# Kernel tuning notes

Measured on AMD Instinct MI355X. Metric: run time of the kernel, lower is better.

Reference implementation:

```python
import jax, jax.numpy as jnp
import numpy as np

NUM_GROUPS = 32
NUM_FEATURES = 256
EPS = 1e-5


def setup_inputs() -> dict:
    key = jax.random.key(0)
    x = jax.random.normal(key, (32, NUM_FEATURES, 64, 64), dtype=jnp.float32)
    gamma = jnp.ones((NUM_FEATURES,), jnp.float32)
    beta = jnp.zeros((NUM_FEATURES,), jnp.float32)
    return {"x": x, "gamma": gamma, "beta": beta}


def reference(x, gamma, beta):
    B, C, H, W = x.shape
    k = NUM_FEATURES // NUM_GROUPS  # channels per dynamic group
    # --- cosine similarity across channels (training path) ---
    x_flat = x.reshape(B, C, H * W)
    nrm = jnp.linalg.norm(x_flat, axis=2, keepdims=True)
    x_n = x_flat / jnp.maximum(nrm, 1e-12)  # F.normalize semantics
    cos = jnp.einsum('bcn,bdn->cd', x_n, x_n) / B  # mean over batch, [C,C]
    # torch.topk(|cos|, k, dim=0, largest=False): per-column k smallest.
    # Row c of |cos|.T is column c, so lax.top_k of -|cos|.T gives idx[c,i]=top_inds[i,c].
    _, idx = jax.lax.top_k(-jnp.abs(cos).T, k)  # [C, k]
    # --- group statistics without materializing [B,C,k,H,W] ---
    s = x.sum(axis=(2, 3))          # [B,C] per-channel spatial sum
    sq = (x * x).sum(axis=(2, 3))   # [B,C]
    # group = channel c itself + channels idx[c,1:]  (idx[:,0] replaced by x in original)
    gs = s + s[:, idx[:, 1:]].sum(axis=-1)    # [B,C]
    gsq = sq + sq[:, idx[:, 1:]].sum(axis=-1)  # [B,C]
    N = k * H * W
    mean = gs / N
    var = gsq / N - mean * mean  # unbiased=False
    inv = jax.lax.rsqrt(var + EPS)
    x_hat = (x - mean[:, :, None, None]) * inv[:, :, None, None]
    return gamma[None, :, None, None] * x_hat + beta[None, :, None, None]
```

## Files before the change

kernel.cpp:

```cpp
#include <hip/hip_runtime.h>
#include <math.h>

#define BATCH 32
#define CH 256
#define HW 4096
#define KSEL 8
#define EPSV 1e-5f

typedef __attribute__((ext_vector_type(8))) short short8;
typedef __attribute__((ext_vector_type(4))) float f32x4;

__global__ __launch_bounds__(1024) void gram256(const float* __restrict__ x,
                                                float* __restrict__ cosP,
                                                float* __restrict__ sP,
                                                float* __restrict__ sqP) {
    int z = blockIdx.x;
    int b = z >> 3, q = z & 7;
    const float* xb = x + (size_t)b * CH * HW;

    __shared__ unsigned short Hh[2][CH * 64];
    __shared__ unsigned short Hl[2][CH * 64];

    int t = threadIdx.x, lane = t & 63, w = t >> 6;
    int wr = (w >> 2) * 64, wc = (w & 3) * 64;
    int fr = lane & 15, fg = lane >> 4;

    int rowbase = t >> 4;
    int col16 = t & 15;
    int gr = col16 >> 1;
    int halfo = (col16 & 1) * 4;
    const float4* srcb4 = (const float4*)xb + (size_t)rowbase * (HW / 4) + q * 128 + col16;

    float sl[4] = {}, sql[4] = {};
    f32x4 acc[4][4] = {};
    float4 f[4];

#define LOAD4(KB) { const float4* sp = srcb4 + (size_t)(KB) * 16;                  \
    _Pragma("unroll") for (int i = 0; i < 4; ++i) f[i] = sp[(size_t)i * 65536]; }

#define CONVERT4(BUF) { _Pragma("unroll") for (int i = 0; i < 4; ++i) {            \
    float4 v = f[i];                                                               \
    sl[i] += v.x + v.y + v.z + v.w;                                                \
    sql[i] += v.x * v.x + v.y * v.y + v.z * v.z + v.w * v.w;                       \
    unsigned u0 = __float_as_uint(v.x), u1 = __float_as_uint(v.y);                 \
    unsigned u2 = __float_as_uint(v.z), u3 = __float_as_uint(v.w);                 \
    unsigned hp0 = (u0 >> 16) | (u1 & 0xffff0000u);                                \
    unsigned hp1 = (u2 >> 16) | (u3 & 0xffff0000u);                                \
    float lo0 = v.x - __uint_as_float(u0 & 0xffff0000u);                           \
    float lo1 = v.y - __uint_as_float(u1 & 0xffff0000u);                           \
    float lo2 = v.z - __uint_as_float(u2 & 0xffff0000u);                           \
    float lo3 = v.w - __uint_as_float(u3 & 0xffff0000u);                           \
    lo0 += lo0; lo1 += lo1; lo2 += lo2; lo3 += lo3;                                \
    unsigned lp0 = (__float_as_uint(lo0) >> 16) | (__float_as_uint(lo1) & 0xffff0000u); \
    unsigned lp1 = (__float_as_uint(lo2) >> 16) | (__float_as_uint(lo3) & 0xffff0000u); \
    int r = rowbase + 64 * i;                                                      \
    int adr = r * 64 + ((gr ^ (r & 7)) * 8) + halfo;                               \
    *(uint2*)&Hh[BUF][adr] = make_uint2(hp0, hp1);                                 \
    *(uint2*)&Hl[BUF][adr] = make_uint2(lp0, lp1);                                 \
} }

#define MFMA_PHASE(BUF) { _Pragma("unroll") for (int ks = 0; ks < 2; ++ks) {       \
    int gk = ks * 4 + fg;                                                          \
    short8 af[4], bb[4];                                                           \
    _Pragma("unroll") for (int mi = 0; mi < 4; ++mi) {                             \
        int r = wr + mi * 16 + fr;                                                 \
        af[mi] = *(const short8*)&Hh[BUF][r * 64 + ((gk ^ (r & 7)) * 8)];          \
    }                                                                              \
    _Pragma("unroll") for (int nj = 0; nj < 4; ++nj) {                             \
        int r = wc + nj * 16 + fr;                                                 \
        bb[nj] = *(const short8*)&Hh[BUF][r * 64 + ((gk ^ (r & 7)) * 8)];          \
    }                                                                              \
    _Pragma("unroll") for (int nj = 0; nj < 4; ++nj)                               \
        _Pragma("unroll") for (int mi = 0; mi < 4; ++mi)                           \
            acc[mi][nj] = __builtin_amdgcn_mfma_f32_16x16x32_bf16(af[mi], bb[nj], acc[mi][nj], 0, 0, 0); \
    _Pragma("unroll") for (int nj = 0; nj < 4; ++nj) {                             \
        int r = wc + nj * 16 + fr;                                                 \
        bb[nj] = *(const short8*)&Hl[BUF][r * 64 + ((gk ^ (r & 7)) * 8)];          \
    }                                                                              \
    _Pragma("unroll") for (int nj = 0; nj < 4; ++nj)                               \
        _Pragma("unroll") for (int mi = 0; mi < 4; ++mi)                           \
            acc[mi][nj] = __builtin_amdgcn_mfma_f32_16x16x32_bf16(af[mi], bb[nj], acc[mi][nj], 0, 0, 0); \
} }

    LOAD4(0)

#pragma unroll 1
    for (int kb = 0; kb < 8; ++kb) {
        CONVERT4(kb & 1)
        if (kb < 7) LOAD4(kb + 1)
        asm volatile("s_waitcnt lgkmcnt(0)" ::: "memory");
        __builtin_amdgcn_sched_barrier(0);
        __builtin_amdgcn_s_barrier();
        MFMA_PHASE(kb & 1)
    }

#pragma unroll
    for (int i = 0; i < 4; ++i) {
#pragma unroll
        for (int off = 1; off < 16; off <<= 1) {
            sl[i] += __shfl_xor(sl[i], off);
            sql[i] += __shfl_xor(sql[i], off);
        }
    }
    if ((t & 15) == 0) {
#pragma unroll
        for (int i = 0; i < 4; ++i) {
            int r = rowbase + 64 * i;
            sP[(size_t)z * CH + r] = sl[i];
            sqP[(size_t)z * CH + r] = sql[i];
        }
    }

    float* Cp = cosP + (size_t)z * CH * CH;
#pragma unroll
    for (int mi = 0; mi < 4; ++mi)
#pragma unroll
        for (int nj = 0; nj < 4; ++nj) {
#pragma unroll
            for (int reg = 0; reg < 4; ++reg) {
                int r = wr + mi * 16 + fg * 4 + reg;
                int c = wc + nj * 16 + fr;
                Cp[(size_t)r * CH + c] = acc[mi][nj][reg];
            }
        }
#undef LOAD4
#undef CONVERT4
#undef MFMA_PHASE
}

__global__ __launch_bounds__(256) void finalize_kernel(const float* __restrict__ sP,
                                                       const float* __restrict__ sqP,
                                                       float* __restrict__ s,
                                                       float* __restrict__ sq,
                                                       float* __restrict__ invn) {
    int b = blockIdx.x, c = threadIdx.x;
    float S = 0.f, Q = 0.f;
#pragma unroll
    for (int q = 0; q < 8; ++q) {
        S += sP[(size_t)(b * 8 + q) * CH + c];
        Q += sqP[(size_t)(b * 8 + q) * CH + c];
    }
    s[b * CH + c] = S;
    sq[b * CH + c] = Q;
    invn[b * CH + c] = 1.0f / fmaxf(sqrtf(Q), 1e-12f);
}

__global__ __launch_bounds__(1024) void reduceP(const float* __restrict__ cosP,
                                                const float* __restrict__ invn,
                                                float* __restrict__ R) {
    int r = blockIdx.x;
    int t = threadIdx.x;
    int d = t & 255, pg = t >> 8;
    const float* base = cosP + (size_t)r * CH + d;
    float acc = 0.f;
    for (int b = pg * 8; b < pg * 8 + 8; ++b) {
        float part = 0.f;
#pragma unroll
        for (int q = 0; q < 8; ++q)
            part += base[(size_t)(b * 8 + q) * (CH * CH)];
        acc += part * invn[b * CH + d] * invn[b * CH + r];
    }
    __shared__ float red[1024];
    red[t] = acc;
    __syncthreads();
    if (t < 256)
        R[(size_t)r * CH + t] = red[t] + red[t + 256] + red[t + 512] + red[t + 768];
}

__global__ __launch_bounds__(256) void symtopk(const float* __restrict__ R,
                                               int* __restrict__ idx) {
    int c = blockIdx.x;
    int d = threadIdx.x;
    float v = fabsf((R[(size_t)c * CH + d] + R[(size_t)d * CH + c]) * (0.5f / BATCH));

    __shared__ unsigned long long keys[CH];
    __shared__ unsigned long long wmin[4];
    __shared__ unsigned long long bmin;

    keys[d] = ((unsigned long long)__float_as_uint(v) << 32) | (unsigned)d;
    __syncthreads();

    for (int i = 0; i < KSEL; ++i) {
        unsigned long long k = keys[d];
        for (int off = 32; off; off >>= 1) {
            unsigned long long o = __shfl_down(k, off);
            k = (o < k) ? o : k;
        }
        if ((d & 63) == 0) wmin[d >> 6] = k;
        __syncthreads();
        if (d == 0) {
            unsigned long long m = wmin[0];
            if (wmin[1] < m) m = wmin[1];
            if (wmin[2] < m) m = wmin[2];
            if (wmin[3] < m) m = wmin[3];
            bmin = m;
            idx[c * KSEL + i] = (int)(m & 0xffffffffu);
        }
        __syncthreads();
        int sel = (int)(bmin & 0xffffffffu);
        if (d == sel) keys[d] = 0xffffffffffffffffULL;
        __syncthreads();
    }
}

__global__ __launch_bounds__(256) void groupstat_kernel(const float* __restrict__ s,
                                                        const float* __restrict__ sq,
                                                        const int* __restrict__ idx,
                                                        float* __restrict__ mean,
                                                        float* __restrict__ inv) {
    int b = blockIdx.x, c = threadIdx.x;
    float gs = s[b * CH + c], gq = sq[b * CH + c];
#pragma unroll
    for (int i = 1; i < KSEL; ++i) {
        int d = idx[c * KSEL + i];
        gs += s[b * CH + d];
        gq += sq[b * CH + d];
    }
    const float Ninv = 1.0f / (float)(KSEL * HW);
    float m = gs * Ninv;
    float var = gq * Ninv - m * m;
    mean[b * CH + c] = m;
    inv[b * CH + c]  = rsqrtf(var + EPSV);
}

__global__ __launch_bounds__(256) void norm_kernel(const float* __restrict__ x,
                                                   const float* __restrict__ mean,
                                                   const float* __restrict__ inv,
                                                   const float* __restrict__ gamma,
                                                   const float* __restrict__ beta,
                                                   float* __restrict__ out) {
    int i = blockIdx.x * 256 + threadIdx.x;
    int bc = i >> 10;
    int c  = bc & (CH - 1);
    float m = mean[bc], v = inv[bc];
    float g  = gamma[c] * v;
    float bt = beta[c] - m * g;
    float4 xv = ((const float4*)x)[i];
    float4 o;
    o.x = xv.x * g + bt;
    o.y = xv.y * g + bt;
    o.z = xv.z * g + bt;
    o.w = xv.w * g + bt;
    ((float4*)out)[i] = o;
}

extern "C" void kernel_launch(void* const* d_in, const int* in_sizes, int n_in,
                              void* d_out, int out_size, void* d_ws, size_t ws_size,
                              hipStream_t stream) {
    const float* x     = (const float*)d_in[0];
    const float* gamma = (const float*)d_in[1];
    const float* beta  = (const float*)d_in[2];
    float* out = (float*)d_out;

    float* cosP = (float*)d_out;

    float* ws   = (float*)d_ws;
    float* sP   = ws;
    float* sqP  = sP + 256 * CH;
    float* s    = sqP + 256 * CH;
    float* sq   = s + BATCH * CH;
    float* invn = sq + BATCH * CH;
    float* mean = invn + BATCH * CH;
    float* inv  = mean + BATCH * CH;
    float* R    = inv + BATCH * CH;
    int*   idx  = (int*)(R + CH * CH);

    gram256<<<256, 1024, 0, stream>>>(x, cosP, sP, sqP);
    finalize_kernel<<<BATCH, 256, 0, stream>>>(sP, sqP, s, sq, invn);
    reduceP<<<CH, 1024, 0, stream>>>(cosP, invn, R);
    symtopk<<<CH, 256, 0, stream>>>(R, idx);
    groupstat_kernel<<<BATCH, 256, 0, stream>>>(s, sq, idx, mean, inv);
    norm_kernel<<<(BATCH * CH * HW / 4) / 256, 256, 0, stream>>>(x, mean, inv, gamma, beta, out);
}
```

Measured before the change: 103.2 us.

## Stage gram inputs via global_load_lds double buffer with padded bf16 tiles

The gram kernel now fetches input through direct global-to-LDS loads into a double-buffered fp32 staging area instead of register loads. Each block converts from LDS into single-buffered hi/lo bf16 tiles, using a padded row stride of 40 in place of the XOR swizzle. The K step is halved to 32, giving 16 iterations. This is meant to overlap global fetch with MFMA work and cut register pressure, at the cost of an extra barrier per iteration and an extra LDS round trip.

Result: slower. 109.7 us (+6.3%).

```diff
diff --git a/kernel.cpp b/kernel.cpp
--- a/kernel.cpp
+++ b/kernel.cpp
@@ -9,6 +9,11 @@
 
 typedef __attribute__((ext_vector_type(8))) short short8;
 typedef __attribute__((ext_vector_type(4))) float f32x4;
+
+__device__ __forceinline__ void gload16(const void* g, void* l) {
+    __builtin_amdgcn_global_load_lds((const __attribute__((address_space(1))) void*)g,
+                                     (__attribute__((address_space(3))) void*)l, 16, 0, 0);
+}
 
 __global__ __launch_bounds__(1024) void gram256(const float* __restrict__ x,
                                                 float* __restrict__ cosP,
@@ -17,31 +22,33 @@
     int z = blockIdx.x;
     int b = z >> 3, q = z & 7;
     const float* xb = x + (size_t)b * CH * HW;
-
-    __shared__ unsigned short Hh[2][CH * 64];
-    __shared__ unsigned short Hl[2][CH * 64];
+    int kbase = q * 512;
+
+    __shared__ float4 ldsF[2][2048];
+    __shared__ unsigned short Hh[CH * 40];
+    __shared__ unsigned short Hl[CH * 40];
 
     int t = threadIdx.x, lane = t & 63, w = t >> 6;
     int wr = (w >> 2) * 64, wc = (w & 3) * 64;
     int fr = lane & 15, fg = lane >> 4;
 
-    int rowbase = t >> 4;
-    int col16 = t & 15;
-    int gr = col16 >> 1;
-    int halfo = (col16 & 1) * 4;
-    const float4* srcb4 = (const float4*)xb + (size_t)rowbase * (HW / 4) + q * 128 + col16;
-
-    float sl[4] = {}, sql[4] = {};
+    int rl = lane >> 3;
+    int gs = lane & 7;
+
+    float sl[2] = {}, sql[2] = {};
     f32x4 acc[4][4] = {};
-    float4 f[4];
-
-#define LOAD4(KB) { const float4* sp = srcb4 + (size_t)(KB) * 16;                  \
-    _Pragma("unroll") for (int i = 0; i < 4; ++i) f[i] = sp[(size_t)i * 65536]; }
-
-#define CONVERT4(BUF) { _Pragma("unroll") for (int i = 0; i < 4; ++i) {            \
-    float4 v = f[i];                                                               \
-    sl[i] += v.x + v.y + v.z + v.w;                                                \
-    sql[i] += v.x * v.x + v.y * v.y + v.z * v.z + v.w * v.w;                       \
+
+#define ISSUE(KB, BUF) { int k0 = kbase + (KB) * 32;                               \
+    _Pragma("unroll") for (int j = 0; j < 2; ++j) {                                \
+        int row = (w * 2 + j) * 8 + rl;                                            \
+        gload16(xb + (size_t)row * HW + k0 + gs * 4, &ldsF[BUF][(w * 2 + j) * 64]); \
+    } }
+
+#define CONVERT(BUF) { _Pragma("unroll") for (int j = 0; j < 2; ++j) {             \
+    float4 v = ldsF[BUF][(w * 2 + j) * 64 + lane];                                 \
+    int r = (w * 2 + j) * 8 + rl;                                                  \
+    sl[j] += v.x + v.y + v.z + v.w;                                                \
+    sql[j] += v.x * v.x + v.y * v.y + v.z * v.z + v.w * v.w;                       \
     unsigned u0 = __float_as_uint(v.x), u1 = __float_as_uint(v.y);                 \
     unsigned u2 = __float_as_uint(v.z), u3 = __float_as_uint(v.w);                 \
     unsigned hp0 = (u0 >> 16) | (u1 & 0xffff0000u);                                \
@@ -53,61 +60,60 @@
     lo0 += lo0; lo1 += lo1; lo2 += lo2; lo3 += lo3;                                \
     unsigned lp0 = (__float_as_uint(lo0) >> 16) | (__float_as_uint(lo1) & 0xffff0000u); \
     unsigned lp1 = (__float_as_uint(lo2) >> 16) | (__float_as_uint(lo3) & 0xffff0000u); \
-    int r = rowbase + 64 * i;                                                      \
-    int adr = r * 64 + ((gr ^ (r & 7)) * 8) + halfo;                               \
-    *(uint2*)&Hh[BUF][adr] = make_uint2(hp0, hp1);                                 \
-    *(uint2*)&Hl[BUF][adr] = make_uint2(lp0, lp1);                                 \
+    int adr = r * 40 + gs * 4;                                                     \
+    *(uint2*)&Hh[adr] = make_uint2(hp0, hp1);                                      \
+    *(uint2*)&Hl[adr] = make_uint2(lp0, lp1);                                      \
 } }
 
-#define MFMA_PHASE(BUF) { _Pragma("unroll") for (int ks = 0; ks < 2; ++ks) {       \
-    int gk = ks * 4 + fg;                                                          \
+#define MFMA_PHASE {                                                               \
     short8 af[4], bb[4];                                                           \
-    _Pragma("unroll") for (int mi = 0; mi < 4; ++mi) {                             \
-        int r = wr + mi * 16 + fr;                                                 \
-        af[mi] = *(const short8*)&Hh[BUF][r * 64 + ((gk ^ (r & 7)) * 8)];          \
-    }                                                                              \
-    _Pragma("unroll") for (int nj = 0; nj < 4; ++nj) {                             \
-        int r = wc + nj * 16 + fr;                                                 \
-        bb[nj] = *(const short8*)&Hh[BUF][r * 64 + ((gk ^ (r & 7)) * 8)];          \
-    }                                                                              \
+    _Pragma("unroll") for (int mi = 0; mi < 4; ++mi)                               \
+        af[mi] = *(const short8*)&Hh[(wr + mi * 16 + fr) * 40 + fg * 8];           \
+    _Pragma("unroll") for (int nj = 0; nj < 4; ++nj)                               \
+        bb[nj] = *(const short8*)&Hh[(wc + nj * 16 + fr) * 40 + fg * 8];           \
     _Pragma("unroll") for (int nj = 0; nj < 4; ++nj)                               \
         _Pragma("unroll") for (int mi = 0; mi < 4; ++mi)                           \
             acc[mi][nj] = __builtin_amdgcn_mfma_f32_16x16x32_bf16(af[mi], bb[nj], acc[mi][nj], 0, 0, 0); \
-    _Pragma("unroll") for (int nj = 0; nj < 4; ++nj) {                             \
-        int r = wc + nj * 16 + fr;                                                 \
-        bb[nj] = *(const short8*)&Hl[BUF][r * 64 + ((gk ^ (r & 7)) * 8)];          \
-    }                                                                              \
+    _Pragma("unroll") for (int nj = 0; nj < 4; ++nj)                               \
+        bb[nj] = *(const short8*)&Hl[(wc + nj * 16 + fr) * 40 + fg * 8];           \
     _Pragma("unroll") for (int nj = 0; nj < 4; ++nj)                               \
         _Pragma("unroll") for (int mi = 0; mi < 4; ++mi)                           \
             acc[mi][nj] = __builtin_amdgcn_mfma_f32_16x16x32_bf16(af[mi], bb[nj], acc[mi][nj], 0, 0, 0); \
-} }
-
-    LOAD4(0)
+}
+
+    ISSUE(0, 0)
+    asm volatile("s_waitcnt vmcnt(0)" ::: "memory");
+    __builtin_amdgcn_sched_barrier(0);
+    __builtin_amdgcn_s_barrier();
 
 #pragma unroll 1
-    for (int kb = 0; kb < 8; ++kb) {
-        CONVERT4(kb & 1)
-        if (kb < 7) LOAD4(kb + 1)
+    for (int kb = 0; kb < 16; ++kb) {
+        if (kb < 15) ISSUE(kb + 1, (kb + 1) & 1)
+        CONVERT(kb & 1)
         asm volatile("s_waitcnt lgkmcnt(0)" ::: "memory");
         __builtin_amdgcn_sched_barrier(0);
         __builtin_amdgcn_s_barrier();
-        MFMA_PHASE(kb & 1)
-    }
-
-#pragma unroll
-    for (int i = 0; i < 4; ++i) {
-#pragma unroll
-        for (int off = 1; off < 16; off <<= 1) {
-            sl[i] += __shfl_xor(sl[i], off);
-            sql[i] += __shfl_xor(sql[i], off);
-        }
-    }
-    if ((t & 15) == 0) {
-#pragma unroll
-        for (int i = 0; i < 4; ++i) {
-            int r = rowbase + 64 * i;
-            sP[(size_t)z * CH + r] = sl[i];
-            sqP[(size_t)z * CH + r] = sql[i];
+        __builtin_amdgcn_sched_barrier(0);
+        MFMA_PHASE
+        asm volatile("s_waitcnt vmcnt(0)" ::: "memory");
+        __builtin_amdgcn_sched_barrier(0);
+        __builtin_amdgcn_s_barrier();
+    }
+
+#pragma unroll
+    for (int j = 0; j < 2; ++j) {
+#pragma unroll
+        for (int off = 1; off < 8; off <<= 1) {
+            sl[j] += __shfl_xor(sl[j], off);
+            sql[j] += __shfl_xor(sql[j], off);
+        }
+    }
+    if (gs == 0) {
+#pragma unroll
+        for (int j = 0; j < 2; ++j) {
+            int r = (w * 2 + j) * 8 + rl;
+            sP[(size_t)z * CH + r] = sl[j];
+            sqP[(size_t)z * CH + r] = sql[j];
         }
     }
 
@@ -123,8 +129,8 @@
                 Cp[(size_t)r * CH + c] = acc[mi][nj][reg];
             }
         }
-#undef LOAD4
-#undef CONVERT4
+#undef ISSUE
+#undef CONVERT
 #undef MFMA_PHASE
 }
 
```
